# Kernel tuning notes

Measured on AMD Instinct MI355X. Metric: run time of the kernel, lower is better.

Reference implementation:

```python
import jax, jax.numpy as jnp
import numpy as np

D_MODEL = 512
N_HEADS = 8
D_HEAD = D_MODEL // N_HEADS
N_BINS = 32


def setup_inputs() -> dict:
    key = jax.random.key(0)
    ks = jax.random.split(key, 12)
    B, N = 8, 1024
    x = jax.random.normal(ks[0], (B, N, D_MODEL), dtype=jnp.float32)
    positions = jax.random.randint(ks[1], (B, N), 0, 5000, dtype=jnp.int32)
    mask = jnp.ones((B, N), dtype=jnp.float32)
    s = 0.02
    qw = jax.random.normal(ks[2], (D_MODEL, D_MODEL), jnp.float32) * s
    qb = jnp.zeros((D_MODEL,), jnp.float32)
    kw = jax.random.normal(ks[3], (D_MODEL, D_MODEL), jnp.float32) * s
    kb = jnp.zeros((D_MODEL,), jnp.float32)
    vw = jax.random.normal(ks[4], (D_MODEL, D_MODEL), jnp.float32) * s
    vb = jnp.zeros((D_MODEL,), jnp.float32)
    ow = jax.random.normal(ks[5], (D_MODEL, D_MODEL), jnp.float32) * s
    ob = jnp.zeros((D_MODEL,), jnp.float32)
    dist_emb = jax.random.normal(ks[6], (N_BINS, N_HEADS), jnp.float32) * s
    order_bias = jnp.zeros((N_HEADS,), jnp.float32)
    bin_edges = jnp.logspace(0.0, 3.0, N_BINS - 1, dtype=jnp.float32)
    return {"x": x, "positions": positions, "mask": mask,
            "qw": qw, "qb": qb, "kw": kw, "kb": kb, "vw": vw, "vb": vb,
            "ow": ow, "ob": ob, "dist_emb": dist_emb, "order_bias": order_bias,
            "bin_edges": bin_edges}


def reference(x, positions, mask, qw, qb, kw, kb, vw, vb, ow, ob, dist_emb, order_bias, bin_edges):
    B, N, _ = x.shape
    scale = jnp.sqrt(jnp.float32(D_HEAD))
    # projections (torch Linear: y = x @ W^T + b), split heads -> (B,H,N,Dh)
    q = (x @ qw.T + qb).reshape(B, N, N_HEADS, D_HEAD).transpose(0, 2, 1, 3)
    k = (x @ kw.T + kb).reshape(B, N, N_HEADS, D_HEAD).transpose(0, 2, 1, 3)
    v = (x @ vw.T + vb).reshape(B, N, N_HEADS, D_HEAD).transpose(0, 2, 1, 3)
    scores = jnp.einsum('bhqd,bhkd->bhqk', q, k) / scale  # (B,H,N,N)
    pos = positions.astype(jnp.float32)
    pos_i = pos[:, :, None]   # (B,N,1)
    pos_j = pos[:, None, :]   # (B,1,N)
    dist = jnp.abs(pos_j - pos_i)  # (B,N,N)
    # torch.bucketize(right=False) == searchsorted side='left'
    bins = jnp.clip(jnp.searchsorted(bin_edges, dist, side='left'), 0, N_BINS - 1)
    dist_bias = dist_emb[bins]  # (B,N,N,H)
    scores = scores + dist_bias.transpose(0, 3, 1, 2)
    order_sign = (pos_j > pos_i).astype(scores.dtype) - 0.5  # (B,N,N)
    scores = scores + order_sign[:, None, :, :] * order_bias[None, :, None, None]
    mask_2d = mask[:, None, None, :] * mask[:, None, :, None]  # (B,1,N,N)
    scores = jnp.where(mask_2d == 0, jnp.float32(-1e9), scores)
    attn = jax.nn.softmax(scores, axis=-1)
    attn = jnp.nan_to_num(attn, nan=0.0)
    out = jnp.einsum('bhqk,bhkd->bhqd', attn, v)
    out = out.transpose(0, 2, 1, 3).reshape(B, N, D_MODEL)
    out = out * mask[..., None]
    return out @ ow.T + ob
```

## Files before the change

kernel.cpp:

```cpp
#include <hip/hip_runtime.h>
#include <hip/hip_bf16.h>

#define SEQ   1024
#define NH    8
#define DH    64

typedef __attribute__((ext_vector_type(8))) _Float16 half8;
typedef __attribute__((ext_vector_type(4))) _Float16 half4;
typedef __attribute__((ext_vector_type(4))) float    f32x4;

#if __has_builtin(__builtin_amdgcn_exp2f)
#define EXP2F __builtin_amdgcn_exp2f
#else
#define EXP2F exp2f
#endif

__device__ inline unsigned pk2(float a, float b) {
  return __builtin_bit_cast(unsigned, __builtin_amdgcn_cvt_pkrtz(a, b));
}
__device__ inline void swap32(unsigned &a, unsigned &b) {
  asm("v_permlane32_swap_b32 %0, %1" : "+v"(a), "+v"(b));
}
__device__ inline void swap16(unsigned &a, unsigned &b) {
  asm("v_permlane16_swap_b32 %0, %1" : "+v"(a), "+v"(b));
}
__device__ inline half8 mk8(unsigned a, unsigned b, unsigned c, unsigned d) {
  union { unsigned u[4]; half8 h; } x;
  x.u[0] = a; x.u[1] = b; x.u[2] = c; x.u[3] = d;
  return x.h;
}
__device__ __forceinline__ void gload16(const _Float16* g, _Float16* l) {
  __builtin_amdgcn_global_load_lds((const __attribute__((address_space(1))) void*)g,
                                   (__attribute__((address_space(3))) void*)l, 16, 0, 0);
}

#define BARRIER1 do {                                        \
    __builtin_amdgcn_sched_barrier(0);                       \
    asm volatile("s_waitcnt vmcnt(1)" ::: "memory");         \
    __builtin_amdgcn_s_barrier();                            \
    __builtin_amdgcn_sched_barrier(0);                       \
  } while (0)

__global__ void prep_all(const float* __restrict__ x,
                         const float* __restrict__ qw, const float* __restrict__ kw,
                         const float* __restrict__ vw, const float* __restrict__ ow,
                         const float* __restrict__ qb, const float* __restrict__ kb,
                         const float* __restrict__ vb, const float* __restrict__ edges,
                         _Float16* __restrict__ xh, _Float16* __restrict__ wqkvh,
                         _Float16* __restrict__ owh, float* __restrict__ qkvbias,
                         unsigned char* __restrict__ lutd) {
  const int blk = blockIdx.x, tid = threadIdx.x;
  if (blk < 4096) {
    int g = blk * 256 + tid;
    float4 v = reinterpret_cast<const float4*>(x)[g];
    half4 u;
    u[0] = (_Float16)v.x; u[1] = (_Float16)v.y; u[2] = (_Float16)v.z; u[3] = (_Float16)v.w;
    reinterpret_cast<half4*>(xh)[g] = u;
  } else if (blk < 5122) {
    int g = (blk - 4096) * 256 + tid;
    if (g < 196608) {
      const float* src = (g < 65536) ? qw : (g < 131072) ? kw : vw;
      int lg = g & 65535;
      float4 v = reinterpret_cast<const float4*>(src)[lg];
      half4 u;
      u[0] = (_Float16)v.x; u[1] = (_Float16)v.y; u[2] = (_Float16)v.z; u[3] = (_Float16)v.w;
      reinterpret_cast<half4*>(wqkvh)[g] = u;
    } else if (g < 262144) {
      int lg = g - 196608;
      float4 v = reinterpret_cast<const float4*>(ow)[lg];
      half4 u;
      u[0] = (_Float16)v.x; u[1] = (_Float16)v.y; u[2] = (_Float16)v.z; u[3] = (_Float16)v.w;
      reinterpret_cast<half4*>(owh)[lg] = u;
    } else if (g < 262528) {
      int lg = g - 262144;
      const float* src = (lg < 128) ? qb : (lg < 256) ? kb : vb;
      int ll = lg & 127;
      reinterpret_cast<float4*>(qkvbias)[lg] = reinterpret_cast<const float4*>(src)[ll];
    }
  } else {
    int d = (blk - 5122) * 256 + tid;
    float fd = (float)d;
    int bin = 0;
#pragma unroll
    for (int t = 0; t < 31; ++t) bin += (edges[t] < fd) ? 1 : 0;
    lutd[d] = (unsigned char)bin;
  }
}

__global__ __launch_bounds__(256) void prep_ebins(const int* __restrict__ positions,
                                                  const float* __restrict__ mask,
                                                  const unsigned char* __restrict__ lutd,
                                                  unsigned char* __restrict__ ebins) {
  __shared__ unsigned char lutl[5120];
  __shared__ int posl[SEQ];
  __shared__ unsigned char mk[SEQ];
  const int b = blockIdx.x >> 8, j0 = (blockIdx.x & 255) * 4;
  const int tid = threadIdx.x;
  for (int i = tid; i < 1280; i += 256)
    reinterpret_cast<unsigned*>(lutl)[i] = reinterpret_cast<const unsigned*>(lutd)[i];
  for (int i = tid; i < SEQ; i += 256) {
    posl[i] = positions[b * SEQ + i];
    mk[i] = (mask[b * SEQ + i] == 0.f) ? 32 : 0;
  }
  __syncthreads();
  const int c0 = tid * 4;
  const int widx = (tid >> 4) * 16 + (tid & 3) * 4 + ((tid >> 2) & 3);
#pragma unroll
  for (int jj = 0; jj < 4; ++jj) {
    const int j = j0 + jj;
    const int pr = posl[j];
    unsigned out = 0;
#pragma unroll
    for (int r = 0; r < 4; ++r) {
      int c = c0 + r;
      int pc = posl[c];
      int d = pc - pr; d = d < 0 ? -d : d;
      if (d > 5119) d = 5119;
      unsigned e = lutl[d] | (unsigned)mk[c] | ((pc > pr) ? 64u : 0u);
      out |= e << (8 * r);
    }
    reinterpret_cast<unsigned*>(&ebins[(size_t)(b * SEQ + j) * SEQ])[widx] = out;
  }
}

__global__ __launch_bounds__(256) void qkv_gemm3(const _Float16* __restrict__ xh,
                                                 const _Float16* __restrict__ wh,
                                                 const float* __restrict__ bias,
                                                 _Float16* __restrict__ qkv) {
  __shared__ __attribute__((aligned(16))) _Float16 As[128 * 64];
  __shared__ __attribute__((aligned(16))) _Float16 Bs[128 * 64];
  const int m0 = blockIdx.x * 128, n0 = blockIdx.y * 128;
  const int tid = threadIdx.x, w = tid >> 6, lane = tid & 63;
  const int lr = lane & 15, lg = lane >> 4;
  const int wr = (w >> 1) * 64, wc = (w & 1) * 64;
  f32x4 acc[4][4] = {};
  const int srow8 = lane >> 3;
  const int scol = ((lane & 7) ^ srow8) * 8;
  for (int k0 = 0; k0 < 512; k0 += 64) {
#pragma unroll
    for (int j = 0; j < 4; ++j) {
      const int row = (w * 4 + j) * 8 + srow8;
      gload16(&xh[(size_t)(m0 + row) * 512 + k0 + scol], &As[(w * 4 + j) * 512]);
      gload16(&wh[(size_t)(n0 + row) * 512 + k0 + scol], &Bs[(w * 4 + j) * 512]);
    }
    __syncthreads();
#pragma unroll
    for (int kk = 0; kk < 2; ++kk) {
      half8 af[4], bf[4];
#pragma unroll
      for (int mt = 0; mt < 4; ++mt) {
        const int row = wr + mt * 16 + lr;
        af[mt] = *reinterpret_cast<const half8*>(
            (const char*)As + row * 128 + (((kk * 4 + lg) ^ (row & 7)) * 16));
      }
#pragma unroll
      for (int nt = 0; nt < 4; ++nt) {
        const int row = wc + nt * 16 + lr;
        bf[nt] = *reinterpret_cast<const half8*>(
            (const char*)Bs + row * 128 + (((kk * 4 + lg) ^ (row & 7)) * 16));
      }
#pragma unroll
      for (int mt = 0; mt < 4; ++mt)
#pragma unroll
        for (int nt = 0; nt < 4; ++nt)
          acc[mt][nt] = __builtin_amdgcn_mfma_f32_16x16x32_f16(af[mt], bf[nt], acc[mt][nt], 0, 0, 0);
    }
    __syncthreads();
  }
  const int p = n0 >> 9;
  const float scl = (p == 0) ? 0.125f : (p == 1) ? 1.44269504f : 1.0f;
  if (p < 2) {
#pragma unroll
    for (int nt = 0; nt < 4; ++nt) {
      int n = n0 + wc + nt * 16 + lr;
      float bv = bias[n];
      int c = n & 511, h = c >> 6, d = c & 63;
#pragma unroll
      for (int mt = 0; mt < 4; ++mt)
#pragma unroll
        for (int r = 0; r < 4; ++r) {
          int m = m0 + wr + mt * 16 + lg * 4 + r;
          int bb = m >> 10, nn = m & 1023;
          qkv[p * 4194304 + ((bb * NH + h) * SEQ + nn) * DH + d] = (_Float16)((acc[mt][nt][r] + bv) * scl);
        }
    }
  } else {
#pragma unroll
    for (int nt = 0; nt < 4; ++nt) {
      int n = n0 + wc + nt * 16 + lr;
      float bv = bias[n];
      int c = n & 511, h = c >> 6, d = c & 63;
#pragma unroll
      for (int mt = 0; mt < 4; ++mt) {
        int m = m0 + wr + mt * 16 + lg * 4;
        int bb = m >> 10, nn = m & 1023;
        half4 st;
#pragma unroll
        for (int r = 0; r < 4; ++r) st[r] = (_Float16)(acc[mt][nt][r] + bv);
        *reinterpret_cast<half4*>(&qkv[8388608 + ((bb * NH + h) * DH + d) * SEQ + nn]) = st;
      }
    }
  }
}

#define ASTAGE(bufi, kv0_) do {                                                              \
    _Pragma("unroll") for (int j = 0; j < 2; ++j) {                                          \
      const int row_ = (w * 2 + j) * 8 + (lane >> 3);                                        \
      const int c_ = ((lane & 7) ^ (row_ & 7)) * 8;                                          \
      gload16(Kg + (size_t)((kv0_) + row_) * 64 + c_, &Ks[bufi][(w * 2 + j) * 512]);         \
      gload16(Vtg + (size_t)row_ * 1024 + (kv0_) + c_, &Vt[bufi][(w * 2 + j) * 512]);        \
    }                                                                                        \
  } while (0)

#define EBL(dst, kt_) do {                                                                   \
    uint4 e4_ = *reinterpret_cast<const uint4*>(                                             \
        &ebins[(size_t)(b * SEQ + q_base + lr) * SEQ + (kt_) * 64 + lg * 16]);               \
    dst[0] = e4_.x; dst[1] = e4_.y; dst[2] = e4_.z; dst[3] = e4_.w;                          \
  } while (0)

#define ACOMP(bufi, ebw) do {                                                                \
    f32x4 s[4];                                                                              \
    _Pragma("unroll") for (int ct = 0; ct < 4; ++ct) {                                       \
      const unsigned eb_ = ebw[ct];                                                          \
      _Pragma("unroll") for (int r = 0; r < 4; ++r) {                                        \
        const unsigned i6_ = (eb_ >> (8 * r)) & 63u;                      \
        float bias_ = elut2[i6_];                                                            \
        if (obh_nz) bias_ += ((eb_ >> (8 * r)) & 64u) ? obh : -obh;                          \
        s[ct][r] = bias_;                                                                    \
      }                                                                                      \
    }                                                                                        \
    __builtin_amdgcn_s_setprio(1);                                                           \
    _Pragma("unroll") for (int ct = 0; ct < 4; ++ct) {                                       \
      const int krow_ = ct * 16 + lr;                                                        \
      half8 kf0 = *reinterpret_cast<const half8*>(                                           \
          (const char*)&Ks[bufi][0] + krow_ * 128 + ((lg ^ (krow_ & 7)) * 16));              \
      half8 kf1 = *reinterpret_cast<const half8*>(                                           \
          (const char*)&Ks[bufi][0] + krow_ * 128 + (((4 + lg) ^ (krow_ & 7)) * 16));        \
      s[ct] = __builtin_amdgcn_mfma_f32_16x16x32_f16(kf0, qf[0], s[ct], 0, 0, 0);            \
      s[ct] = __builtin_amdgcn_mfma_f32_16x16x32_f16(kf1, qf[1], s[ct], 0, 0, 0);            \
    }                                                                                        \
    __builtin_amdgcn_s_setprio(0);                                                           \
                 \
    unsigned W[4][2];                                                                        \
    _Pragma("unroll") for (int ct = 0; ct < 4; ++ct) {                                       \
      float p0 = EXP2F(s[ct][0]), p1 = EXP2F(s[ct][1]);                                      \
      float p2 = EXP2F(s[ct][2]), p3 = EXP2F(s[ct][3]);                                      \
      l_run += (p0 + p1) + (p2 + p3);                                                        \
      W[ct][0] = pk2(p0, p1);                                                                \
      W[ct][1] = pk2(p2, p3);                                                                \
    }                                                                                        \
    swap32(W[0][0], W[1][0]); swap32(W[0][1], W[1][1]);                                      \
    swap32(W[2][0], W[3][0]); swap32(W[2][1], W[3][1]);                                      \
    swap16(W[0][0], W[1][0]); swap16(W[0][1], W[1][1]);                                      \
    swap16(W[2][0], W[3][0]); swap16(W[2][1], W[3][1]);                                      \
    __builtin_amdgcn_s_setprio(1);                                                           \
    _Pragma("unroll") for (int ks = 0; ks < 2; ++ks) {                                       \
      half8 pa = mk8(W[ks * 2][0], W[ks * 2][1], W[ks * 2 + 1][0], W[ks * 2 + 1][1]);        \
      _Pragma("unroll") for (int dt = 0; dt < 4; ++dt) {                                     \
        const int vrow_ = dt * 16 + lr;                                                      \
        half8 vf = *reinterpret_cast<const half8*>(                                          \
            (const char*)&Vt[bufi][0] + vrow_ * 128 + (((ks * 4 + lg) ^ (vrow_ & 7)) * 16)); \
        o[dt] = __builtin_amdgcn_mfma_f32_16x16x32_f16(vf, pa, o[dt], 0, 0, 0);              \
      }                                                                                      \
    }                                                                                        \
    __builtin_amdgcn_s_setprio(0);                                                           \
  } while (0)

__global__ __launch_bounds__(256, 4) void attn11(const _Float16* __restrict__ qkv,
                                                 const float* __restrict__ mask,
                                                 const unsigned char* __restrict__ ebins,
                                                 const float* __restrict__ demb,
                                                 const float* __restrict__ obias,
                                                 _Float16* __restrict__ aout) {
  __shared__ __attribute__((aligned(16))) _Float16 Ks[2][64 * 64];
  __shared__ __attribute__((aligned(16))) _Float16 Vt[2][64 * 64];
  __shared__ float elut2[64];

  const int blk = blockIdx.x;
  const int lin = (blk & 7) * 128 + (blk >> 3);
  const int qt = lin & 15, h = (lin >> 4) & 7, b = lin >> 7;
  const int tid = threadIdx.x, w = tid >> 6, lane = tid & 63;
  const int lr = lane & 15, lg = lane >> 4;

  if (tid < 64) elut2[tid] = (tid < 32) ? demb[tid * NH + h] * 1.44269504f : -1.442695e9f;
  const float obh = 0.5f * obias[h] * 1.44269504f;
  const bool obh_nz = (obh != 0.f);

  const _Float16* Qg  = qkv + (size_t)(b * NH + h) * 65536;
  const _Float16* Kg  = qkv + 4194304 + (size_t)(b * NH + h) * 65536;
  const _Float16* Vtg = qkv + 8388608 + (size_t)(b * NH + h) * 65536;

  const int q_base = qt * 64 + w * 16;
  half8 qf[2];
#pragma unroll
  for (int ks = 0; ks < 2; ++ks)
    qf[ks] = *reinterpret_cast<const half8*>(&Qg[(q_base + lr) * DH + ks * 32 + lg * 8]);
  const float mq = mask[b * SEQ + q_base + lr];

  float l_run = 0.f;
  f32x4 o[4] = {};

  unsigned ebwA[4], ebwB[4];
  ASTAGE(0, 0);
  EBL(ebwA, 0);
  __syncthreads();

#pragma unroll 1
  for (int i = 0; i < 8; ++i) {
    const int kt = 2 * i;
    ASTAGE(1, (kt + 1) * 64);
    EBL(ebwB, kt + 1);
    ACOMP(0, ebwA);
    BARRIER1;
    if (kt + 2 < 16) {
      ASTAGE(0, (kt + 2) * 64);
      EBL(ebwA, kt + 2);
    }
    ACOMP(1, ebwB);
    BARRIER1;
  }

  float s_ = l_run;
  s_ += __shfl_xor(s_, 16);
  s_ += __shfl_xor(s_, 32);
  const float linv = mq / fmaxf(s_, 1e-35f);
#pragma unroll
  for (int dt = 0; dt < 4; ++dt) {
    half4 st;
#pragma unroll
    for (int r = 0; r < 4; ++r) st[r] = (_Float16)(o[dt][r] * linv);
    *reinterpret_cast<half4*>(
        &aout[(size_t)(b * SEQ + q_base + lr) * 512 + h * DH + dt * 16 + lg * 4]) = st;
  }
}

__global__ __launch_bounds__(256) void out_gemm3(const _Float16* __restrict__ ah,
                                                 const _Float16* __restrict__ wh,
                                                 const float* __restrict__ ob,
                                                 float* __restrict__ out) {
  __shared__ __attribute__((aligned(16))) _Float16 As[128 * 64];
  __shared__ __attribute__((aligned(16))) _Float16 Bs[64 * 64];
  const int m0 = blockIdx.x * 128, n0 = blockIdx.y * 64;
  const int tid = threadIdx.x, w = tid >> 6, lane = tid & 63;
  const int lr = lane & 15, lg = lane >> 4;
  const int wr = (w >> 1) * 64, wc = (w & 1) * 32;
  f32x4 acc[4][2] = {};
  const int srow8 = lane >> 3;
  const int scol = ((lane & 7) ^ srow8) * 8;
  for (int k0 = 0; k0 < 512; k0 += 64) {
#pragma unroll
    for (int j = 0; j < 4; ++j) {
      const int row = (w * 4 + j) * 8 + srow8;
      gload16(&ah[(size_t)(m0 + row) * 512 + k0 + scol], &As[(w * 4 + j) * 512]);
    }
#pragma unroll
    for (int j = 0; j < 2; ++j) {
      const int row = (w * 2 + j) * 8 + srow8;
      gload16(&wh[(size_t)(n0 + row) * 512 + k0 + scol], &Bs[(w * 2 + j) * 512]);
    }
    __syncthreads();
#pragma unroll
    for (int kk = 0; kk < 2; ++kk) {
      half8 af[4], bf[2];
#pragma unroll
      for (int mt = 0; mt < 4; ++mt) {
        const int row = wr + mt * 16 + lr;
        af[mt] = *reinterpret_cast<const half8*>(
            (const char*)As + row * 128 + (((kk * 4 + lg) ^ (row & 7)) * 16));
      }
#pragma unroll
      for (int nt = 0; nt < 2; ++nt) {
        const int row = wc + nt * 16 + lr;
        bf[nt] = *reinterpret_cast<const half8*>(
            (const char*)Bs + row * 128 + (((kk * 4 + lg) ^ (row & 7)) * 16));
      }
#pragma unroll
      for (int mt = 0; mt < 4; ++mt)
#pragma unroll
        for (int nt = 0; nt < 2; ++nt)
          acc[mt][nt] = __builtin_amdgcn_mfma_f32_16x16x32_f16(af[mt], bf[nt], acc[mt][nt], 0, 0, 0);
    }
    __syncthreads();
  }
#pragma unroll
  for (int nt = 0; nt < 2; ++nt) {
    int n = n0 + wc + nt * 16 + lr;
    float bv = ob[n];
#pragma unroll
    for (int mt = 0; mt < 4; ++mt)
#pragma unroll
      for (int r = 0; r < 4; ++r) {
        int m = m0 + wr + mt * 16 + lg * 4 + r;
        out[m * 512 + n] = acc[mt][nt][r] + bv;
      }
  }
}

extern "C" void kernel_launch(void* const* d_in, const int* in_sizes, int n_in,
                              void* d_out, int out_size, void* d_ws, size_t ws_size,
                              hipStream_t stream) {
  const float* x         = (const float*)d_in[0];
  const int*   positions = (const int*)d_in[1];
  const float* mask      = (const float*)d_in[2];
  const float* qw        = (const float*)d_in[3];
  const float* qb        = (const float*)d_in[4];
  const float* kw        = (const float*)d_in[5];
  const float* kb        = (const float*)d_in[6];
  const float* vw        = (const float*)d_in[7];
  const float* vb        = (const float*)d_in[8];
  const float* ow        = (const float*)d_in[9];
  const float* ob        = (const float*)d_in[10];
  const float* demb      = (const float*)d_in[11];
  const float* obias     = (const float*)d_in[12];
  const float* edges     = (const float*)d_in[13];

  char* ws = (char*)d_ws;
  _Float16* xh        = (_Float16*)(ws);
  unsigned char* ebins = (unsigned char*)(ws);
  _Float16* qkv       = (_Float16*)(ws + 8388608);
  _Float16* aouth     = (_Float16*)(ws + 33554432);
  _Float16* wqkvh     = (_Float16*)(ws + 41943040);
  _Float16* owh       = (_Float16*)(ws + 43515904);
  float*    qkvbias   = (float*)(ws + 44040192);
  unsigned char* lutd = (unsigned char*)(ws + 44046336);
  float*    outp      = (float*)d_out;

  prep_all<<<5142, 256, 0, stream>>>(x, qw, kw, vw, ow, qb, kb, vb, edges,
                                     xh, wqkvh, owh, qkvbias, lutd);
  qkv_gemm3<<<dim3(64, 12), 256, 0, stream>>>(xh, wqkvh, qkvbias, qkv);
  prep_ebins<<<2048, 256, 0, stream>>>(positions, mask, lutd, ebins);
  attn11<<<1024, 256, 0, stream>>>(qkv, mask, ebins, demb, obias, aouth);
  out_gemm3<<<dim3(64, 8), 256, 0, stream>>>(aouth, owh, ob, outp);
}
```

Before: 95.16 us.

## Load K fragments directly from global into registers instead of LDS

The attention kernel no longer stages K tiles through shared memory. Each wave loads its K MFMA fragments straight from global memory into double-buffered registers, and the vmcnt waits are adjusted for the extra outstanding loads. This removes the LDS round trip and LDS reads for K. In exchange, each wave redundantly loads the same K tile, and register pressure rises, which may limit occupancy.

```diff
diff --git a/kernel.cpp b/kernel.cpp
--- a/kernel.cpp
+++ b/kernel.cpp
@@ -34,9 +34,11 @@
                                    (__attribute__((address_space(3))) void*)l, 16, 0, 0);
 }
 
-#define BARRIER1 do {                                        \
+#define SB0 __builtin_amdgcn_sched_barrier(0)
+
+#define BARRIER9 do {                                        \
     __builtin_amdgcn_sched_barrier(0);                       \
-    asm volatile("s_waitcnt vmcnt(1)" ::: "memory");         \
+    asm volatile("s_waitcnt vmcnt(9)" ::: "memory");         \
     __builtin_amdgcn_s_barrier();                            \
     __builtin_amdgcn_sched_barrier(0);                       \
   } while (0)
@@ -203,12 +205,20 @@
   }
 }
 
-#define ASTAGE(bufi, kv0_) do {                                                              \
+#define ASTAGEV(bufi, kv0_) do {                                                             \
     _Pragma("unroll") for (int j = 0; j < 2; ++j) {                                          \
       const int row_ = (w * 2 + j) * 8 + (lane >> 3);                                        \
       const int c_ = ((lane & 7) ^ (row_ & 7)) * 8;                                          \
-      gload16(Kg + (size_t)((kv0_) + row_) * 64 + c_, &Ks[bufi][(w * 2 + j) * 512]);         \
       gload16(Vtg + (size_t)row_ * 1024 + (kv0_) + c_, &Vt[bufi][(w * 2 + j) * 512]);        \
+    }                                                                                        \
+  } while (0)
+
+#define KLOAD(dst, kt_) do {                                                                 \
+    const int kv0_ = (kt_) * 64;                                                             \
+    _Pragma("unroll") for (int ct = 0; ct < 4; ++ct) {                                       \
+      const size_t kro_ = (size_t)(kv0_ + ct * 16 + lr) * 64;                                \
+      dst[ct * 2 + 0] = *reinterpret_cast<const half8*>(&Kg[kro_ + lg * 8]);                 \
+      dst[ct * 2 + 1] = *reinterpret_cast<const half8*>(&Kg[kro_ + 32 + lg * 8]);            \
     }                                                                                        \
   } while (0)
 
@@ -218,7 +228,7 @@
     dst[0] = e4_.x; dst[1] = e4_.y; dst[2] = e4_.z; dst[3] = e4_.w;                          \
   } while (0)
 
-#define ACOMP(bufi, ebw) do {                                                                \
+#define ACOMP(bufi, ebw, kf) do {                                                            \
     f32x4 s[4];                                                                              \
     _Pragma("unroll") for (int ct = 0; ct < 4; ++ct) {                                       \
       const unsigned eb_ = ebw[ct];                                                          \
@@ -231,13 +241,8 @@
     }                                                                                        \
     __builtin_amdgcn_s_setprio(1);                                                           \
     _Pragma("unroll") for (int ct = 0; ct < 4; ++ct) {                                       \
-      const int krow_ = ct * 16 + lr;                                                        \
-      half8 kf0 = *reinterpret_cast<const half8*>(                                           \
-          (const char*)&Ks[bufi][0] + krow_ * 128 + ((lg ^ (krow_ & 7)) * 16));              \
-      half8 kf1 = *reinterpret_cast<const half8*>(                                           \
-          (const char*)&Ks[bufi][0] + krow_ * 128 + (((4 + lg) ^ (krow_ & 7)) * 16));        \
-      s[ct] = __builtin_amdgcn_mfma_f32_16x16x32_f16(kf0, qf[0], s[ct], 0, 0, 0);            \
-      s[ct] = __builtin_amdgcn_mfma_f32_16x16x32_f16(kf1, qf[1], s[ct], 0, 0, 0);            \
+      s[ct] = __builtin_amdgcn_mfma_f32_16x16x32_f16(kf[ct * 2 + 0], qf[0], s[ct], 0, 0, 0); \
+      s[ct] = __builtin_amdgcn_mfma_f32_16x16x32_f16(kf[ct * 2 + 1], qf[1], s[ct], 0, 0, 0); \
     }                                                                                        \
     __builtin_amdgcn_s_setprio(0);                                                           \
                  \
@@ -266,13 +271,12 @@
     __builtin_amdgcn_s_setprio(0);                                                           \
   } while (0)
 
-__global__ __launch_bounds__(256, 4) void attn11(const _Float16* __restrict__ qkv,
+__global__ __launch_bounds__(256, 4) void attn12(const _Float16* __restrict__ qkv,
                                                  const float* __restrict__ mask,
                                                  const unsigned char* __restrict__ ebins,
                                                  const float* __restrict__ demb,
                                                  const float* __restrict__ obias,
                                                  _Float16* __restrict__ aout) {
-  __shared__ __attribute__((aligned(16))) _Float16 Ks[2][64 * 64];
   __shared__ __attribute__((aligned(16))) _Float16 Vt[2][64 * 64];
   __shared__ float elut2[64];
 
@@ -300,24 +304,32 @@
   float l_run = 0.f;
   f32x4 o[4] = {};
 
+  half8 kfA[8], kfB[8];
   unsigned ebwA[4], ebwB[4];
-  ASTAGE(0, 0);
+  ASTAGEV(0, 0);
+  KLOAD(kfA, 0);
   EBL(ebwA, 0);
   __syncthreads();
 
 #pragma unroll 1
   for (int i = 0; i < 8; ++i) {
     const int kt = 2 * i;
-    ASTAGE(1, (kt + 1) * 64);
+    ASTAGEV(1, (kt + 1) * 64);
+    SB0;
+    KLOAD(kfB, kt + 1);
     EBL(ebwB, kt + 1);
-    ACOMP(0, ebwA);
-    BARRIER1;
+    SB0;
+    ACOMP(0, ebwA, kfA);
+    BARRIER9;
     if (kt + 2 < 16) {
-      ASTAGE(0, (kt + 2) * 64);
+      ASTAGEV(0, (kt + 2) * 64);
+      SB0;
+      KLOAD(kfA, kt + 2);
       EBL(ebwA, kt + 2);
-    }
-    ACOMP(1, ebwB);
-    BARRIER1;
+      SB0;
+    }
+    ACOMP(1, ebwB, kfB);
+    BARRIER9;
   }
 
   float s_ = l_run;
@@ -429,6 +441,6 @@
                                      xh, wqkvh, owh, qkvbias, lutd);
   qkv_gemm3<<<dim3(64, 12), 256, 0, stream>>>(xh, wqkvh, qkvbias, qkv);
   prep_ebins<<<2048, 256, 0, stream>>>(positions, mask, lutd, ebins);
-  attn11<<<1024, 256, 0, stream>>>(qkv, mask, ebins, demb, obias, aouth);
+  attn12<<<1024, 256, 0, stream>>>(qkv, mask, ebins, demb, obias, aouth);
   out_gemm3<<<dim3(64, 8), 256, 0, stream>>>(aouth, owh, ob, outp);
 }
```

New measurement: 153.4 us. 61.2% more time.
